# Optimization experiments

Measured on AMD Instinct MI355X. Metric: run time of the kernel, lower is better.

Reference implementation:

```python
import jax, jax.numpy as jnp
import numpy as np

B, S, D, H = 2, 2048, 1024, 16
HD = D // H


def setup_inputs() -> dict:
    key = jax.random.key(0)
    ks = jax.random.split(key, 6)
    scale = D ** -0.5
    return {
        "x": jax.random.normal(ks[0], (B, S, D), dtype=jnp.float32),
        "attn_mask": jnp.ones((B, S), dtype=bool),
        "wq": jax.random.normal(ks[1], (D, D), dtype=jnp.float32) * scale,
        "wk": jax.random.normal(ks[2], (D, D), dtype=jnp.float32) * scale,
        "wv": jax.random.normal(ks[3], (D, D), dtype=jnp.float32) * scale,
        "wo": jax.random.normal(ks[4], (D, D), dtype=jnp.float32) * scale,
        "bo": jax.random.normal(ks[5], (D,), dtype=jnp.float32) * 0.01,
    }


def reference(x, attn_mask, wq, wk, wv, wo, bo):
    b, s, d = x.shape
    # torch Linear: y = x @ W.T
    q = (x @ wq.T).reshape(b, s, H, HD).transpose(0, 2, 1, 3)  # (b,h,s,hd)
    k = (x @ wk.T).reshape(b, s, H, HD).transpose(0, 2, 1, 3)
    v = (x @ wv.T).reshape(b, s, H, HD).transpose(0, 2, 1, 3)
    scores = jnp.einsum("bhqd,bhkd->bhqk", q, k) * (HD ** -0.5)
    causal = jnp.triu(jnp.ones((s, s), dtype=bool), k=1)  # True above diagonal
    mask = causal[None, None, :, :] | (~attn_mask)[:, None, None, :]
    mask_value = jnp.finfo(scores.dtype).min / 2
    scores = jnp.where(mask, mask_value, scores)
    att = jax.nn.softmax(scores, axis=-1)
    ctx = jnp.einsum("bhqk,bhkd->bhqd", att, v)
    ctx = ctx.transpose(0, 2, 1, 3).reshape(b, s, d)
    return ctx @ wo.T + bo
```

## Files before the change

### kernel.cpp

```cpp
#include <hip/hip_runtime.h>
#include <stdint.h>

#define SEQ   2048
#define DMODEL 1024
#define NHEAD 16
#define HDIM  64
#define MTOT  4096

typedef short s16x8 __attribute__((ext_vector_type(8)));
typedef float f32x4 __attribute__((ext_vector_type(4)));
typedef float f32x16 __attribute__((ext_vector_type(16)));
typedef unsigned u32x4 __attribute__((ext_vector_type(4)));

#define LOG2E 1.44269504088896340736f

#if __has_builtin(__builtin_amdgcn_exp2f)
#define EXP2(x) __builtin_amdgcn_exp2f(x)
#else
#define EXP2(x) exp2f(x)
#endif

__device__ __forceinline__ short f2bf(float f) {
  union { float f; unsigned u; } v; v.f = f;
  unsigned u = v.u + 0x7fff + ((v.u >> 16) & 1);
  return (short)(u >> 16);
}

__device__ __forceinline__ void async_cp16(const void* g, void* l) {
  __builtin_amdgcn_global_load_lds(
      (const __attribute__((address_space(1))) void*)g,
      (__attribute__((address_space(3))) void*)l, 16, 0, 0);
}

__device__ __forceinline__ f32x4 mfma16(s16x8 a, s16x8 b, f32x4 c) {
  return __builtin_amdgcn_mfma_f32_16x16x32_bf16(a, b, c, 0, 0, 0);
}
__device__ __forceinline__ f32x16 mfma32(s16x8 a, s16x8 b, f32x16 c) {
  return __builtin_amdgcn_mfma_f32_32x32x16_bf16(a, b, c, 0, 0, 0);
}

__global__ __launch_bounds__(256) void cast_kernel(
    const float* __restrict__ x,  const float* __restrict__ wq,
    const float* __restrict__ wk, const float* __restrict__ wv,
    const float* __restrict__ wo,
    short* __restrict__ xb,  short* __restrict__ wqb,
    short* __restrict__ wkb, short* __restrict__ wvb, short* __restrict__ wob) {
  int i = blockIdx.x * 256 + threadIdx.x;
  const float4* src; short* dst; int off;
  const int XN = 1 << 20, WN = 1 << 18;
  if (i < XN)            { src = (const float4*)x;  dst = xb;  off = i; }
  else if (i < XN + WN)  { src = (const float4*)wq; dst = wqb; off = i - XN; }
  else if (i < XN + 2*WN){ src = (const float4*)wk; dst = wkb; off = i - XN - WN; }
  else if (i < XN + 3*WN){ src = (const float4*)wv; dst = wvb; off = i - XN - 2*WN; }
  else                   { src = (const float4*)wo; dst = wob; off = i - XN - 3*WN; }
  float4 v = src[off];
  short4 o; o.x = f2bf(v.x); o.y = f2bf(v.y); o.z = f2bf(v.z); o.w = f2bf(v.w);
  *(short4*)(dst + off * 4) = o;
}

__global__ __launch_bounds__(256, 3) void qkv_gemm(
    const short* __restrict__ xb,  const short* __restrict__ wqb,
    const short* __restrict__ wkb, const short* __restrict__ wvb,
    short* __restrict__ Q, short* __restrict__ K, short* __restrict__ Vt) {
  __shared__ short Abuf[2][128 * 32];
  __shared__ short Bbuf[2][128 * 32];
  const int tid = threadIdx.x;
  const int w = tid >> 6, lane = tid & 63;
  const int c = lane & 15, g = lane >> 4;
  const int wm = w >> 1, wn = w & 1;
  const int n0 = blockIdx.x * 128, m0 = blockIdx.y * 128;
  const int z = blockIdx.z;
  const short* __restrict__ W = (z == 0) ? wqb : (z == 1 ? wkb : wvb);
  const int srow = lane >> 2, schunk = lane & 3;

  f32x4 acc[4][4] = {};

#define QKV_STAGE(KT, BS)                                                      \
  _Pragma("unroll") for (int j = 0; j < 2; ++j) {                              \
    int p = w * 2 + j;                                                         \
    async_cp16(xb + (m0 + p * 16 + srow) * 1024 + (KT) * 32 + schunk * 8,      \
               &Abuf[BS][p * 512]);                                            \
    async_cp16(W + (n0 + p * 16 + srow) * 1024 + (KT) * 32 + schunk * 8,       \
               &Bbuf[BS][p * 512]);                                            \
  }

  QKV_STAGE(0, 0)
  for (int kt = 0; kt < 32; ++kt) {
    __syncthreads();
    if (kt + 1 < 32) { QKV_STAGE(kt + 1, (kt + 1) & 1) }
    const int cur = kt & 1;
    s16x8 a[4], b[4];
#pragma unroll
    for (int t = 0; t < 4; ++t)
      a[t] = *(const s16x8*)&Abuf[cur][(wm * 64 + t * 16 + c) * 32 + g * 8];
#pragma unroll
    for (int u = 0; u < 4; ++u)
      b[u] = *(const s16x8*)&Bbuf[cur][(wn * 64 + u * 16 + c) * 32 + g * 8];
#pragma unroll
    for (int t = 0; t < 4; ++t)
#pragma unroll
      for (int u = 0; u < 4; ++u)
        acc[t][u] = mfma16(a[t], b[u], acc[t][u]);
  }

  if (z == 2) {
#pragma unroll
    for (int t = 0; t < 4; ++t)
#pragma unroll
      for (int u = 0; u < 4; ++u) {
        int col = n0 + wn * 64 + u * 16 + c;
        int h = col >> 6, hd = col & 63;
        int m = m0 + wm * 64 + t * 16 + g * 4;
        int b = m >> 11, s = m & 2047;
        short4 o;
        o.x = f2bf(acc[t][u][0]); o.y = f2bf(acc[t][u][1]);
        o.z = f2bf(acc[t][u][2]); o.w = f2bf(acc[t][u][3]);
        *(short4*)&Vt[((b * 16 + h) * 64 + hd) * 2048 + s] = o;
      }
  } else {
    short* __restrict__ dst = (z == 0) ? Q : K;
    const float scale = (z == 0) ? 0.125f * LOG2E : 1.0f;
#pragma unroll
    for (int t = 0; t < 4; ++t)
#pragma unroll
      for (int u = 0; u < 4; ++u) {
        int col = n0 + wn * 64 + u * 16 + c;
        int h = col >> 6, hd = col & 63;
#pragma unroll
        for (int r = 0; r < 4; ++r) {
          int m = m0 + wm * 64 + t * 16 + g * 4 + r;
          int b = m >> 11, s = m & 2047;
          dst[((b * 16 + h) * 2048 + s) * 64 + hd] = f2bf(acc[t][u][r] * scale);
        }
      }
  }
}

#define STAGE_K(KT, BS)                                                        \
  _Pragma("unroll") for (int j = 0; j < 4; ++j) {                              \
    int idx = w * 4 + j;                                                       \
    int ks = idx >> 3, p = idx & 7;                                            \
    async_cp16(Kg + ((KT) * 128 + p * 16 + srow) * 64 + ks * 32 + sw8,         \
               &Kbuf[BS][ks][p * 512]);                                        \
  }
#define STAGE_V(KT)                                                            \
  _Pragma("unroll") for (int j = 0; j < 4; ++j) {                              \
    int idx = w * 4 + j;                                                       \
    int ks2 = idx >> 2, p = idx & 3;                                           \
    async_cp16(Vg + (p * 16 + srow) * 2048 + (KT) * 128 + ks2 * 32 + sw8,      \
               &Vlds[ks2][p * 512]);                                           \
  }

__global__ __launch_bounds__(256, 3) void attn_kernel(
    const short* __restrict__ Q, const short* __restrict__ K,
    const short* __restrict__ Vt, short* __restrict__ ctx) {
  __shared__ short Kbuf[2][2][128 * 32];
  __shared__ short Vlds[4][64 * 32];
  __shared__ float Llds[4][32];

  const int tid = threadIdx.x;
  const int w = tid >> 6, lane = tid & 63;
  const int n31 = lane & 31, h = lane >> 5;
  int bx = blockIdx.x;
  if (blockIdx.y >= 16) bx = 15 - bx;
  const int bh = blockIdx.y;
  const int qbase = bx * 128 + w * 32;
  const short* __restrict__ Qg = Q + bh * (SEQ * HDIM);
  const short* __restrict__ Kg = K + bh * (SEQ * HDIM);
  const short* __restrict__ Vg = Vt + bh * (SEQ * HDIM);
  const int srow = lane >> 2, schunk = lane & 3;
  const int sw8 = (schunk ^ ((srow >> 1) & 3)) * 8;
  const int rsw = (n31 >> 1) & 3;

  s16x8 qf[4];
#pragma unroll
  for (int ch = 0; ch < 4; ++ch)
    qf[ch] = *(const s16x8*)&Qg[(qbase + n31) * 64 + ch * 16 + h * 8];

  float l_run = 0.f;
  f32x16 oacc[2] = {};

  STAGE_K(0, 0)
  for (int kt = 0; kt <= bx; ++kt) {
    __syncthreads();
    if (kt < bx) { STAGE_K(kt + 1, (kt + 1) & 1) }
    STAGE_V(kt)

    const bool diag = (kt == bx);
    const int mtmax = diag ? w : 3;
    const short (*Kc)[128 * 32] = Kbuf[kt & 1];

    unsigned pk[4][8];
#pragma unroll
    for (int mt = 0; mt < 4; ++mt) {
      if (mt > mtmax) break;
      f32x16 st = {};
#pragma unroll
      for (int ch = 0; ch < 4; ++ch) {
        s16x8 ka = *(const s16x8*)
            &Kc[ch >> 1][(mt * 32 + n31) * 32 + ((((ch & 1) * 2 + h) ^ rsw) * 8)];
        st = mfma32(ka, qf[ch], st);
      }
      if (diag && mt == w) {
#pragma unroll
        for (int reg = 0; reg < 16; ++reg) {
          int krow = (reg & 3) + 8 * (reg >> 2) + 4 * h;
          if (krow > n31) st[reg] = -1e30f;
        }
      }
#pragma unroll
      for (int i = 0; i < 8; ++i) {
        float p0 = EXP2(st[2 * i]);
        float p1 = EXP2(st[2 * i + 1]);
        unsigned t0 = __float_as_uint(p0) & 0xffff0000u;
        unsigned t1 = __float_as_uint(p1) & 0xffff0000u;
        l_run += __uint_as_float(t0);
        l_run += __uint_as_float(t1);
        pk[mt][i] = (t0 >> 16) | t1;
      }
    }

    __syncthreads();

#pragma unroll
    for (int mt = 0; mt < 4; ++mt) {
      if (mt > mtmax) break;
#pragma unroll
      for (int kb2 = 0; kb2 < 2; ++kb2) {
        const int kb = mt * 2 + kb2;
        const unsigned q0 = pk[mt][kb2 * 4 + 0], q1 = pk[mt][kb2 * 4 + 1];
        const unsigned q2 = pk[mt][kb2 * 4 + 2], q3 = pk[mt][kb2 * 4 + 3];
        const unsigned x0 = __shfl_xor(q0, 32), x1 = __shfl_xor(q1, 32);
        const unsigned x2 = __shfl_xor(q2, 32), x3 = __shfl_xor(q3, 32);
        u32x4 av;
        av.x = h ? x2 : q0;
        av.y = h ? x3 : q1;
        av.z = h ? q2 : x0;
        av.w = h ? q3 : x1;
        s16x8 pa = __builtin_bit_cast(s16x8, av);
#pragma unroll
        for (int u = 0; u < 2; ++u) {
          s16x8 vf = *(const s16x8*)
              &Vlds[kb >> 1][(u * 32 + n31) * 32 + ((((kb & 1) * 2 + h) ^ rsw) * 8)];
          oacc[u] = mfma32(pa, vf, oacc[u]);
        }
      }
    }
  }

  float lf = l_run + __shfl_xor(l_run, 32);
  if (h == 0) Llds[w][n31] = lf;
  float inv[4][4];
#pragma unroll
  for (int gi = 0; gi < 4; ++gi) {
    float4 lv = *(const float4*)&Llds[w][gi * 8 + 4 * h];
    inv[gi][0] = 1.0f / lv.x; inv[gi][1] = 1.0f / lv.y;
    inv[gi][2] = 1.0f / lv.z; inv[gi][3] = 1.0f / lv.w;
  }

  const int b = bh >> 4, hh = bh & 15;
#pragma unroll
  for (int u = 0; u < 2; ++u)
#pragma unroll
    for (int gi = 0; gi < 4; ++gi)
#pragma unroll
      for (int ri = 0; ri < 4; ++ri) {
        int q = qbase + 8 * gi + 4 * h + ri;
        int hd = u * 32 + n31;
        ctx[(b * 2048 + q) * 1024 + hh * 64 + hd] =
            f2bf(oacc[u][gi * 4 + ri] * inv[gi][ri]);
      }
}

__global__ __launch_bounds__(256) void out_gemm(
    const short* __restrict__ ctx, const short* __restrict__ wob,
    const float* __restrict__ bo, float* __restrict__ out) {
  __shared__ short Abuf[2][128 * 32];
  __shared__ short Bbuf[2][64 * 32];
  const int tid = threadIdx.x;
  const int w = tid >> 6, lane = tid & 63;
  const int c = lane & 15, g = lane >> 4;
  const int wm = w >> 1, wn = w & 1;
  const int n0 = blockIdx.x * 64, m0 = blockIdx.y * 128;
  const int srow = lane >> 2, schunk = lane & 3;

  f32x4 acc[4][2] = {};

#define OUT_STAGE(KT, BS)                                                      \
  {                                                                            \
    _Pragma("unroll") for (int j = 0; j < 2; ++j) {                            \
      int p = w * 2 + j;                                                       \
      async_cp16(ctx + (m0 + p * 16 + srow) * 1024 + (KT) * 32 + schunk * 8,   \
                 &Abuf[BS][p * 512]);                                          \
    }                                                                          \
    async_cp16(wob + (n0 + w * 16 + srow) * 1024 + (KT) * 32 + schunk * 8,     \
               &Bbuf[BS][w * 512]);                                            \
  }

  OUT_STAGE(0, 0)
  for (int kt = 0; kt < 32; ++kt) {
    __syncthreads();
    if (kt + 1 < 32) { OUT_STAGE(kt + 1, (kt + 1) & 1) }
    const int cur = kt & 1;
    s16x8 a[4], b[2];
#pragma unroll
    for (int t = 0; t < 4; ++t)
      a[t] = *(const s16x8*)&Abuf[cur][(wm * 64 + t * 16 + c) * 32 + g * 8];
#pragma unroll
    for (int u = 0; u < 2; ++u)
      b[u] = *(const s16x8*)&Bbuf[cur][(wn * 32 + u * 16 + c) * 32 + g * 8];
#pragma unroll
    for (int t = 0; t < 4; ++t)
#pragma unroll
      for (int u = 0; u < 2; ++u)
        acc[t][u] = mfma16(a[t], b[u], acc[t][u]);
  }

#pragma unroll
  for (int t = 0; t < 4; ++t)
#pragma unroll
    for (int u = 0; u < 2; ++u) {
      int col = n0 + wn * 32 + u * 16 + c;
      float bias = bo[col];
#pragma unroll
      for (int r = 0; r < 4; ++r) {
        int m = m0 + wm * 64 + t * 16 + g * 4 + r;
        out[m * 1024 + col] = acc[t][u][r] + bias;
      }
    }
}

extern "C" void kernel_launch(void* const* d_in, const int* in_sizes, int n_in,
                              void* d_out, int out_size, void* d_ws, size_t ws_size,
                              hipStream_t stream) {
  const float* x  = (const float*)d_in[0];
  const float* wq = (const float*)d_in[2];
  const float* wk = (const float*)d_in[3];
  const float* wv = (const float*)d_in[4];
  const float* wo = (const float*)d_in[5];
  const float* bo = (const float*)d_in[6];

  char* ws = (char*)d_ws;
  short* xb  = (short*)(ws);
  short* wqb = (short*)(ws + (size_t)( 8 << 20));
  short* wkb = (short*)(ws + (size_t)(10 << 20));
  short* wvb = (short*)(ws + (size_t)(12 << 20));
  short* wob = (short*)(ws + (size_t)(14 << 20));
  short* Qb  = (short*)(ws + (size_t)(16 << 20));
  short* Kb  = (short*)(ws + (size_t)(24 << 20));
  short* Vtb = (short*)(ws + (size_t)(32 << 20));
  short* ctx = (short*)(ws + (size_t)(40 << 20));
  float* out = (float*)d_out;

  cast_kernel<<<dim3(8192), dim3(256), 0, stream>>>(x, wq, wk, wv, wo,
                                                    xb, wqb, wkb, wvb, wob);
  qkv_gemm<<<dim3(8, 32, 3), dim3(256), 0, stream>>>(xb, wqb, wkb, wvb,
                                                     Qb, Kb, Vtb);
  attn_kernel<<<dim3(16, 32), dim3(256), 0, stream>>>(Qb, Kb, Vtb, ctx);
  out_gemm<<<dim3(16, 32), dim3(256), 0, stream>>>(ctx, wob, bo, out);
}
```

Measured before the change: 183.9 us.

## Stage QKV epilogue through LDS and double-buffer 64-key attention tiles

The QKV GEMM epilogue now writes results into a swizzled shared-memory tile and then issues coalesced 16-byte global stores for Q, K and the transposed V. Previously it wrote scattered 2-byte or 8-byte values straight to global memory. The attention kernel moves from 128-key tiles to 64-key tiles, with K and V both double-buffered and V prefetched one step ahead. This removes the mid-iteration barrier and raises the occupancy hint to 4 blocks. The cost is more loop iterations, each with less work per barrier.

```diff
diff --git a/kernel.cpp b/kernel.cpp
--- a/kernel.cpp
+++ b/kernel.cpp
@@ -62,8 +62,9 @@
     const short* __restrict__ xb,  const short* __restrict__ wqb,
     const short* __restrict__ wkb, const short* __restrict__ wvb,
     short* __restrict__ Q, short* __restrict__ K, short* __restrict__ Vt) {
-  __shared__ short Abuf[2][128 * 32];
-  __shared__ short Bbuf[2][128 * 32];
+  __shared__ short SMEM[16384];
+  short (*Abuf)[4096] = reinterpret_cast<short (*)[4096]>(SMEM);
+  short (*Bbuf)[4096] = reinterpret_cast<short (*)[4096]>(SMEM + 8192);
   const int tid = threadIdx.x;
   const int w = tid >> 6, lane = tid & 63;
   const int c = lane & 15, g = lane >> 4;
@@ -103,59 +104,80 @@
         acc[t][u] = mfma16(a[t], b[u], acc[t][u]);
   }
 
+  __syncthreads();
+  short* E = SMEM;
+  const int b0 = m0 >> 11, sbase = m0 & 2047, hgb = n0 >> 6;
+
   if (z == 2) {
 #pragma unroll
     for (int t = 0; t < 4; ++t)
 #pragma unroll
       for (int u = 0; u < 4; ++u) {
-        int col = n0 + wn * 64 + u * 16 + c;
-        int h = col >> 6, hd = col & 63;
-        int m = m0 + wm * 64 + t * 16 + g * 4;
-        int b = m >> 11, s = m & 2047;
+        int col = wn * 64 + u * 16 + c;
+        int m = wm * 64 + t * 16 + g * 4;
+        int phys = (m >> 3) ^ (col & 15);
         short4 o;
         o.x = f2bf(acc[t][u][0]); o.y = f2bf(acc[t][u][1]);
         o.z = f2bf(acc[t][u][2]); o.w = f2bf(acc[t][u][3]);
-        *(short4*)&Vt[((b * 16 + h) * 64 + hd) * 2048 + s] = o;
-      }
+        *(short4*)&E[col * 128 + phys * 8 + (m & 7)] = o;
+      }
+    __syncthreads();
+#pragma unroll
+    for (int p = 0; p < 8; ++p) {
+      int R = p * 16 + w * 4 + (lane >> 4);
+      int j = lane & 15;
+      int phys = j ^ (R & 15);
+      s16x8 v = *(const s16x8*)&E[R * 128 + phys * 8];
+      int hloc = R >> 6, hd = R & 63;
+      *(s16x8*)&Vt[(((b0 * 16 + hgb + hloc) * 64 + hd) * 2048) + sbase + j * 8] = v;
+    }
   } else {
+    const float scale = (z == 0) ? 0.125f * LOG2E : 1.0f;
+#pragma unroll
+    for (int t = 0; t < 4; ++t)
+#pragma unroll
+      for (int u = 0; u < 4; ++u)
+#pragma unroll
+        for (int r = 0; r < 4; ++r) {
+          int m = wm * 64 + t * 16 + g * 4 + r;
+          int col = wn * 64 + u * 16 + c;
+          int phys = (col >> 3) ^ ((m >> 2) & 15);
+          E[m * 128 + phys * 8 + (col & 7)] = f2bf(acc[t][u][r] * scale);
+        }
+    __syncthreads();
     short* __restrict__ dst = (z == 0) ? Q : K;
-    const float scale = (z == 0) ? 0.125f * LOG2E : 1.0f;
-#pragma unroll
-    for (int t = 0; t < 4; ++t)
-#pragma unroll
-      for (int u = 0; u < 4; ++u) {
-        int col = n0 + wn * 64 + u * 16 + c;
-        int h = col >> 6, hd = col & 63;
-#pragma unroll
-        for (int r = 0; r < 4; ++r) {
-          int m = m0 + wm * 64 + t * 16 + g * 4 + r;
-          int b = m >> 11, s = m & 2047;
-          dst[((b * 16 + h) * 2048 + s) * 64 + hd] = f2bf(acc[t][u][r] * scale);
-        }
-      }
-  }
-}
-
-#define STAGE_K(KT, BS)                                                        \
-  _Pragma("unroll") for (int j = 0; j < 4; ++j) {                              \
-    int idx = w * 4 + j;                                                       \
-    int ks = idx >> 3, p = idx & 7;                                            \
-    async_cp16(Kg + ((KT) * 128 + p * 16 + srow) * 64 + ks * 32 + sw8,         \
+#pragma unroll
+    for (int p = 0; p < 8; ++p) {
+      int R = p * 32 + w * 8 + (lane >> 3);
+      int j = lane & 7;
+      int m = R >> 1, hloc = R & 1;
+      int phys = (hloc * 8 + j) ^ ((m >> 2) & 15);
+      s16x8 v = *(const s16x8*)&E[m * 128 + phys * 8];
+      *(s16x8*)&dst[(((b0 * 16 + hgb + hloc) * 2048) + sbase + m) * 64 + j * 8] = v;
+    }
+  }
+}
+
+#define STAGE_K64(KT, BS)                                                      \
+  _Pragma("unroll") for (int j = 0; j < 2; ++j) {                              \
+    int idx = w * 2 + j;                                                       \
+    int ks = idx >> 2, p = idx & 3;                                            \
+    async_cp16(Kg + ((KT) * 64 + p * 16 + srow) * 64 + ks * 32 + sw8,          \
                &Kbuf[BS][ks][p * 512]);                                        \
   }
-#define STAGE_V(KT)                                                            \
-  _Pragma("unroll") for (int j = 0; j < 4; ++j) {                              \
-    int idx = w * 4 + j;                                                       \
+#define STAGE_V64(KT, BS)                                                      \
+  _Pragma("unroll") for (int j = 0; j < 2; ++j) {                              \
+    int idx = w * 2 + j;                                                       \
     int ks2 = idx >> 2, p = idx & 3;                                           \
-    async_cp16(Vg + (p * 16 + srow) * 2048 + (KT) * 128 + ks2 * 32 + sw8,      \
-               &Vlds[ks2][p * 512]);                                           \
-  }
-
-__global__ __launch_bounds__(256, 3) void attn_kernel(
+    async_cp16(Vg + (p * 16 + srow) * 2048 + (KT) * 64 + ks2 * 32 + sw8,       \
+               &Vlds[BS][ks2][p * 512]);                                       \
+  }
+
+__global__ __launch_bounds__(256, 4) void attn_kernel(
     const short* __restrict__ Q, const short* __restrict__ K,
     const short* __restrict__ Vt, short* __restrict__ ctx) {
-  __shared__ short Kbuf[2][2][128 * 32];
-  __shared__ short Vlds[4][64 * 32];
+  __shared__ short Kbuf[2][2][64 * 32];
+  __shared__ short Vlds[2][2][64 * 32];
   __shared__ float Llds[4][32];
 
   const int tid = threadIdx.x;
@@ -179,21 +201,22 @@
 
   float l_run = 0.f;
   f32x16 oacc[2] = {};
-
-  STAGE_K(0, 0)
-  for (int kt = 0; kt <= bx; ++kt) {
-    __syncthreads();
-    if (kt < bx) { STAGE_K(kt + 1, (kt + 1) & 1) }
-    STAGE_V(kt)
-
-    const bool diag = (kt == bx);
-    const int mtmax = diag ? w : 3;
-    const short (*Kc)[128 * 32] = Kbuf[kt & 1];
-
-    unsigned pk[4][8];
-#pragma unroll
-    for (int mt = 0; mt < 4; ++mt) {
-      if (mt > mtmax) break;
+  const int qb = 4 * bx + w;
+  const int ktmax = 2 * bx + 1;
+
+  STAGE_K64(0, 0) STAGE_V64(0, 0)
+  for (int kt = 0; kt <= ktmax; ++kt) {
+    __syncthreads();
+    if (kt < ktmax) { STAGE_K64(kt + 1, (kt + 1) & 1) STAGE_V64(kt + 1, (kt + 1) & 1) }
+
+    const short (*Kc)[64 * 32] = Kbuf[kt & 1];
+    const short (*Vc)[64 * 32] = Vlds[kt & 1];
+
+    unsigned pk[2][8];
+#pragma unroll
+    for (int mt = 0; mt < 2; ++mt) {
+      const int kk = 2 * kt + mt;
+      if (kk > qb) break;
       f32x16 st = {};
 #pragma unroll
       for (int ch = 0; ch < 4; ++ch) {
@@ -201,7 +224,7 @@
             &Kc[ch >> 1][(mt * 32 + n31) * 32 + ((((ch & 1) * 2 + h) ^ rsw) * 8)];
         st = mfma32(ka, qf[ch], st);
       }
-      if (diag && mt == w) {
+      if (kk == qb) {
 #pragma unroll
         for (int reg = 0; reg < 16; ++reg) {
           int krow = (reg & 3) + 8 * (reg >> 2) + 4 * h;
@@ -220,11 +243,10 @@
       }
     }
 
-    __syncthreads();
-
-#pragma unroll
-    for (int mt = 0; mt < 4; ++mt) {
-      if (mt > mtmax) break;
+#pragma unroll
+    for (int mt = 0; mt < 2; ++mt) {
+      const int kk = 2 * kt + mt;
+      if (kk > qb) break;
 #pragma unroll
       for (int kb2 = 0; kb2 < 2; ++kb2) {
         const int kb = mt * 2 + kb2;
@@ -241,7 +263,7 @@
 #pragma unroll
         for (int u = 0; u < 2; ++u) {
           s16x8 vf = *(const s16x8*)
-              &Vlds[kb >> 1][(u * 32 + n31) * 32 + ((((kb & 1) * 2 + h) ^ rsw) * 8)];
+              &Vc[kb >> 1][(u * 32 + n31) * 32 + ((((kb & 1) * 2 + h) ^ rsw) * 8)];
           oacc[u] = mfma32(pa, vf, oacc[u]);
         }
       }
```

After: 190.6 us. +3.6%, slower.

## Fuse Q/K/V projections into one block sharing A tile, stage stores through LDS

Applied to the files above, without the earlier changes.

The QKV GEMM now computes all three projections in a single 512-thread block, loading each x tile once and reusing it against the wq, wk and wv tiles, instead of launching three separate z-slices that each reload x. The epilogue stages results through swizzled shared memory so Q, K and the transposed V are written with coalesced 16-byte stores rather than scattered 2-byte or 8-byte stores. This cuts redundant x traffic and improves write coalescing. In exchange the grid has a third as many blocks, LDS use rises to 64KB per block, and accumulator register pressure grows.

```diff
diff --git a/kernel.cpp b/kernel.cpp
--- a/kernel.cpp
+++ b/kernel.cpp
@@ -58,30 +58,32 @@
   *(short4*)(dst + off * 4) = o;
 }
 
-__global__ __launch_bounds__(256, 3) void qkv_gemm(
+__global__ __launch_bounds__(512, 2) void qkv_gemm(
     const short* __restrict__ xb,  const short* __restrict__ wqb,
     const short* __restrict__ wkb, const short* __restrict__ wvb,
     short* __restrict__ Q, short* __restrict__ K, short* __restrict__ Vt) {
-  __shared__ short Abuf[2][128 * 32];
-  __shared__ short Bbuf[2][128 * 32];
+  __shared__ short SMEM[32768];
+  short (*Abuf)[4096] = reinterpret_cast<short (*)[4096]>(SMEM);
+  short (*Bbuf)[3][4096] = reinterpret_cast<short (*)[3][4096]>(SMEM + 8192);
   const int tid = threadIdx.x;
   const int w = tid >> 6, lane = tid & 63;
   const int c = lane & 15, g = lane >> 4;
-  const int wm = w >> 1, wn = w & 1;
+  const int wm = w >> 2, wn = w & 3;
   const int n0 = blockIdx.x * 128, m0 = blockIdx.y * 128;
-  const int z = blockIdx.z;
-  const short* __restrict__ W = (z == 0) ? wqb : (z == 1 ? wkb : wvb);
   const int srow = lane >> 2, schunk = lane & 3;
 
-  f32x4 acc[4][4] = {};
+  f32x4 acc[3][4][2] = {};
 
 #define QKV_STAGE(KT, BS)                                                      \
-  _Pragma("unroll") for (int j = 0; j < 2; ++j) {                              \
-    int p = w * 2 + j;                                                         \
-    async_cp16(xb + (m0 + p * 16 + srow) * 1024 + (KT) * 32 + schunk * 8,      \
-               &Abuf[BS][p * 512]);                                            \
-    async_cp16(W + (n0 + p * 16 + srow) * 1024 + (KT) * 32 + schunk * 8,       \
-               &Bbuf[BS][p * 512]);                                            \
+  {                                                                            \
+    async_cp16(xb + (m0 + w * 16 + srow) * 1024 + (KT) * 32 + schunk * 8,      \
+               &Abuf[BS][w * 512]);                                            \
+    async_cp16(wqb + (n0 + w * 16 + srow) * 1024 + (KT) * 32 + schunk * 8,     \
+               &Bbuf[BS][0][w * 512]);                                         \
+    async_cp16(wkb + (n0 + w * 16 + srow) * 1024 + (KT) * 32 + schunk * 8,     \
+               &Bbuf[BS][1][w * 512]);                                         \
+    async_cp16(wvb + (n0 + w * 16 + srow) * 1024 + (KT) * 32 + schunk * 8,     \
+               &Bbuf[BS][2][w * 512]);                                         \
   }
 
   QKV_STAGE(0, 0)
@@ -89,50 +91,78 @@
     __syncthreads();
     if (kt + 1 < 32) { QKV_STAGE(kt + 1, (kt + 1) & 1) }
     const int cur = kt & 1;
-    s16x8 a[4], b[4];
+    s16x8 a[4];
 #pragma unroll
     for (int t = 0; t < 4; ++t)
       a[t] = *(const s16x8*)&Abuf[cur][(wm * 64 + t * 16 + c) * 32 + g * 8];
 #pragma unroll
-    for (int u = 0; u < 4; ++u)
-      b[u] = *(const s16x8*)&Bbuf[cur][(wn * 64 + u * 16 + c) * 32 + g * 8];
-#pragma unroll
-    for (int t = 0; t < 4; ++t)
-#pragma unroll
-      for (int u = 0; u < 4; ++u)
-        acc[t][u] = mfma16(a[t], b[u], acc[t][u]);
-  }
-
-  if (z == 2) {
-#pragma unroll
-    for (int t = 0; t < 4; ++t)
-#pragma unroll
-      for (int u = 0; u < 4; ++u) {
-        int col = n0 + wn * 64 + u * 16 + c;
-        int h = col >> 6, hd = col & 63;
-        int m = m0 + wm * 64 + t * 16 + g * 4;
-        int b = m >> 11, s = m & 2047;
-        short4 o;
-        o.x = f2bf(acc[t][u][0]); o.y = f2bf(acc[t][u][1]);
-        o.z = f2bf(acc[t][u][2]); o.w = f2bf(acc[t][u][3]);
-        *(short4*)&Vt[((b * 16 + h) * 64 + hd) * 2048 + s] = o;
-      }
-  } else {
-    short* __restrict__ dst = (z == 0) ? Q : K;
-    const float scale = (z == 0) ? 0.125f * LOG2E : 1.0f;
-#pragma unroll
-    for (int t = 0; t < 4; ++t)
-#pragma unroll
-      for (int u = 0; u < 4; ++u) {
-        int col = n0 + wn * 64 + u * 16 + c;
-        int h = col >> 6, hd = col & 63;
-#pragma unroll
-        for (int r = 0; r < 4; ++r) {
-          int m = m0 + wm * 64 + t * 16 + g * 4 + r;
-          int b = m >> 11, s = m & 2047;
-          dst[((b * 16 + h) * 2048 + s) * 64 + hd] = f2bf(acc[t][u][r] * scale);
+    for (int z = 0; z < 3; ++z) {
+      s16x8 b[2];
+#pragma unroll
+      for (int u = 0; u < 2; ++u)
+        b[u] = *(const s16x8*)&Bbuf[cur][z][(wn * 32 + u * 16 + c) * 32 + g * 8];
+#pragma unroll
+      for (int t = 0; t < 4; ++t)
+#pragma unroll
+        for (int u = 0; u < 2; ++u)
+          acc[z][t][u] = mfma16(a[t], b[u], acc[z][t][u]);
+    }
+  }
+
+  short* E = SMEM;
+  const int b0 = m0 >> 11, sbase = m0 & 2047, hgb = n0 >> 6;
+
+#pragma unroll
+  for (int z = 0; z < 3; ++z) {
+    __syncthreads();
+    if (z == 2) {
+#pragma unroll
+      for (int t = 0; t < 4; ++t)
+#pragma unroll
+        for (int u = 0; u < 2; ++u) {
+          int col = wn * 32 + u * 16 + c;
+          int m = wm * 64 + t * 16 + g * 4;
+          int phys = (m >> 3) ^ (col & 15);
+          short4 o;
+          o.x = f2bf(acc[z][t][u][0]); o.y = f2bf(acc[z][t][u][1]);
+          o.z = f2bf(acc[z][t][u][2]); o.w = f2bf(acc[z][t][u][3]);
+          *(short4*)&E[col * 128 + phys * 8 + (m & 7)] = o;
         }
-      }
+      __syncthreads();
+#pragma unroll
+      for (int p = 0; p < 4; ++p) {
+        int R = p * 32 + (tid >> 4);
+        int j = tid & 15;
+        int phys = j ^ (R & 15);
+        s16x8 v = *(const s16x8*)&E[R * 128 + phys * 8];
+        int hloc = R >> 6, hd = R & 63;
+        *(s16x8*)&Vt[(((b0 * 16 + hgb + hloc) * 64 + hd) * 2048) + sbase + j * 8] = v;
+      }
+    } else {
+      const float scale = (z == 0) ? 0.125f * LOG2E : 1.0f;
+#pragma unroll
+      for (int t = 0; t < 4; ++t)
+#pragma unroll
+        for (int u = 0; u < 2; ++u)
+#pragma unroll
+          for (int r = 0; r < 4; ++r) {
+            int m = wm * 64 + t * 16 + g * 4 + r;
+            int col = wn * 32 + u * 16 + c;
+            int phys = (col >> 3) ^ ((m >> 2) & 15);
+            E[m * 128 + phys * 8 + (col & 7)] = f2bf(acc[z][t][u][r] * scale);
+          }
+      __syncthreads();
+      short* __restrict__ dst = (z == 0) ? Q : K;
+#pragma unroll
+      for (int p = 0; p < 4; ++p) {
+        int R = p * 64 + (tid >> 3);
+        int j = tid & 7;
+        int m = R >> 1, hloc = R & 1;
+        int phys = (hloc * 8 + j) ^ ((m >> 2) & 15);
+        s16x8 v = *(const s16x8*)&E[m * 128 + phys * 8];
+        *(s16x8*)&dst[(((b0 * 16 + hgb + hloc) * 2048) + sbase + m) * 64 + j * 8] = v;
+      }
+    }
   }
 }
 
@@ -354,8 +384,8 @@
 
   cast_kernel<<<dim3(8192), dim3(256), 0, stream>>>(x, wq, wk, wv, wo,
                                                     xb, wqb, wkb, wvb, wob);
-  qkv_gemm<<<dim3(8, 32, 3), dim3(256), 0, stream>>>(xb, wqb, wkb, wvb,
-                                                     Qb, Kb, Vtb);
+  qkv_gemm<<<dim3(8, 32), dim3(512), 0, stream>>>(xb, wqb, wkb, wvb,
+                                                  Qb, Kb, Vtb);
   attn_kernel<<<dim3(16, 32), dim3(256), 0, stream>>>(Qb, Kb, Vtb, ctx);
   out_gemm<<<dim3(16, 32), dim3(256), 0, stream>>>(ctx, wob, bo, out);
 }
```

After: 183.6 us. Within noise of the previous version (-0.2%).
